# Kernel optimization log

Measured on AMD Instinct MI355X. Metric: run time of the kernel, lower is better.

Reference implementation:

```python
import jax, jax.numpy as jnp
import numpy as np

N, M, G, H, ND, E = 4096, 8192, 8, 128, 16, 131072
MAX_PERIOD = 10000.0


def setup_inputs() -> dict:
    key = jax.random.key(0)
    ks = jax.random.split(key, 24)
    s = 0.05
    inp = {
        "x": jax.random.normal(ks[0], (N, ND), jnp.float32),
        "edge_index": jax.random.randint(ks[1], (2, E), 0, N),
        "timestep": jax.random.randint(ks[2], (G,), 0, 1000),
        "batch_map": jnp.sort(jax.random.randint(ks[3], (N,), 0, G)),
        "obj_nucleotide_mask": jax.random.randint(ks[4], (M,), 0, 3),
        "obj_central_mask": jax.random.bernoulli(ks[5], 0.3, (M,)),
        "obj_backbone_mask": jax.random.bernoulli(ks[6], 0.5, (M,)),
        "obj_x": jax.random.normal(ks[7], (M, ND - 3), jnp.float32),
        "obj_pos": jax.random.normal(ks[8], (M, 3), jnp.float32),
        "obj_batch": jnp.sort(jax.random.randint(ks[9], (M,), 0, G)),
        # params (stored [in, out]; y = x @ W + b)
        "W_node": s * jax.random.normal(ks[10], (ND, H)),
        "b_node": jnp.zeros((H,)),
        "W_cond": s * jax.random.normal(ks[11], (H, H)),
        "b_cond": jnp.zeros((H,)),
        "W_time": s * jax.random.normal(ks[12], (H, H)),
        "b_time": jnp.zeros((H,)),
        "W_conv1": s * jax.random.normal(ks[13], (H, H)),
        "b_conv1": jnp.zeros((H,)),
        "W_conv2": s * jax.random.normal(ks[14], (H, H)),
        "b_conv2": jnp.zeros((H,)),
        "W_out": s * jax.random.normal(ks[15], (H, ND)),
        "b_out": jnp.zeros((ND,)),
        "w_edge": s * jax.random.normal(ks[16], (2 * H,)),
        "b_edge": jnp.zeros(()),
    }
    return inp


def timestep_embedding(t, dim):
    half = dim // 2
    freqs = jnp.exp(-np.log(MAX_PERIOD) * jnp.arange(half, dtype=jnp.float32) / half)
    args = t[:, None].astype(jnp.float32) * freqs[None]
    return jnp.concatenate([jnp.cos(args), jnp.sin(args)], axis=-1)


def gcn_conv(xh, src, dst, norm, W, b, n):
    # x' = D^-1/2 (A+I) D^-1/2 (X W) + b  (PyG GCNConv, self-loops included in src/dst/norm)
    xw = xh @ W
    msg = xw[src] * norm[:, None]
    return jax.ops.segment_sum(msg, dst, num_segments=n) + b


def reference(x, edge_index, timestep, batch_map, obj_nucleotide_mask,
              obj_central_mask, obj_backbone_mask, obj_x, obj_pos, obj_batch,
              W_node, b_node, W_cond, b_cond, W_time, b_time,
              W_conv1, b_conv1, W_conv2, b_conv2, W_out, b_out, w_edge, b_edge):
    n = x.shape[0]
    # timestep embedding + projections
    time_emb = timestep_embedding(timestep, H)            # [G, H]
    node_emb = x @ W_node + b_node                        # [N, H]

    # condition node pooling (masked mean per graph)
    is_left = obj_nucleotide_mask == 0
    is_central = obj_central_mask
    is_right = obj_nucleotide_mask == 2
    is_base = ~obj_backbone_mask
    is_cond = is_left | (is_central & is_base) | (is_right & is_base)  # [M]
    cond_x = jnp.concatenate([obj_x, obj_pos], axis=1)    # [M, ND]
    cond_emb = cond_x @ W_node + b_node                   # [M, H]
    cm = is_cond.astype(cond_emb.dtype)
    sums = jax.ops.segment_sum(cond_emb * cm[:, None], obj_batch, num_segments=G)
    cnt = jax.ops.segment_sum(cm, obj_batch, num_segments=G)
    pooled = sums / jnp.maximum(cnt, 1.0)[:, None]        # [G, H]

    time_h = time_emb @ W_time + b_time                   # [G, H]
    cond_h = pooled @ W_cond + b_cond                     # [G, H]
    node_emb = node_emb + time_h[batch_map] + cond_h[batch_map]

    # GCN normalization with self-loops (shared by both conv layers)
    loop = jnp.arange(n)
    src = jnp.concatenate([edge_index[0], loop])
    dst = jnp.concatenate([edge_index[1], loop])
    deg = jax.ops.segment_sum(jnp.ones_like(src, jnp.float32), dst, num_segments=n)
    dinv = jnp.where(deg > 0, jax.lax.rsqrt(jnp.maximum(deg, 1.0)), 0.0)
    norm = dinv[src] * dinv[dst]

    h = jax.nn.relu(gcn_conv(node_emb, src, dst, norm, W_conv1, b_conv1, n))
    h = jax.nn.relu(gcn_conv(h, src, dst, norm, W_conv2, b_conv2, n))

    node_noise_pred = h @ W_out + b_out                   # [N, ND]

    # all-pairs edge logits: cat([h[row], h[col]]) @ w_edge + b
    # == (h @ w_left)[row] + (h @ w_right)[col] + b  (same math, avoids [P, 2H])
    row, col = jnp.triu_indices(n, k=1)
    s_l = h @ w_edge[:H]
    s_r = h @ w_edge[H:]
    edge_logits = s_l[row] + s_r[col] + b_edge            # [N*(N-1)/2]
    return (node_noise_pred, edge_logits)
```

## Files before the change

### kernel.cpp

```cpp
#include <hip/hip_runtime.h>

#define NN 4096
#define MM 8192
#define GG 8
#define HH 128
#define NDD 16
#define EE 131072
#define CBLK 64
#define COBJ (MM / CBLK)
#define WBLK 8
#define SBLK 128
#define CAP 96

typedef float nt_f4 __attribute__((ext_vector_type(4)));

__global__ __launch_bounds__(1024) void k_zero(int* __restrict__ cnt) {
    ((int4*)cnt)[threadIdx.x] = make_int4(0, 0, 0, 0);
}

__global__ __launch_bounds__(256) void k_front(
    const float* __restrict__ obj_x, const float* __restrict__ obj_pos,
    const int* __restrict__ nuc, const int* __restrict__ central,
    const int* __restrict__ backbone, const int* __restrict__ obj_batch,
    const int* __restrict__ e_src, const int* __restrict__ e_dst,
    int* __restrict__ cnt, int* __restrict__ col_idx,
    float* __restrict__ partial, float* __restrict__ pcnt,
    const float* __restrict__ Wn, const float* __restrict__ Wc1,
    float* __restrict__ W1p) {
    int b = blockIdx.x, t = threadIdx.x;
    if (b < CBLK) {
        __shared__ float ls[GG * NDD];
        __shared__ float lc[GG];
        if (t < GG * NDD) ls[t] = 0.f;
        if (t < GG) lc[t] = 0.f;
        __syncthreads();
        int d = t & 15, oi = t >> 4;
        int base = b * COBJ;
#pragma unroll
        for (int pass = 0; pass < COBJ / 16; pass++) {
            int o = base + pass * 16 + oi;
            int nv = nuc[o];
            bool isb = (backbone[o] == 0);
            bool cond = (nv == 0) || ((central[o] != 0) && isb) || ((nv == 2) && isb);
            if (cond) {
                float v = (d < 13) ? obj_x[o * 13 + d] : obj_pos[o * 3 + (d - 13)];
                int g = obj_batch[o];
                atomicAdd(&ls[g * NDD + d], v);
                if (d == 0) atomicAdd(&lc[g], 1.f);
            }
        }
        __syncthreads();
        if (t < GG * NDD) partial[b * (GG * NDD) + t] = ls[t];
        if (t < GG) pcnt[b * GG + t] = lc[t];
        return;
    }
    if (b < CBLK + WBLK) {
        int wb = b - CBLK;
        int j = t & 127, a0 = t >> 7;
        int a = wb * 2 + a0;
        float acc = 0.f;
        for (int k = 0; k < HH; k++) acc += Wn[a * HH + k] * Wc1[k * HH + j];
        W1p[a * HH + j] = acc;
        return;
    }
    int sb = b - (CBLK + WBLK);
    int i4 = sb * 256 + t;
    int4 d4 = ((const int4*)e_dst)[i4];
    int4 s4 = ((const int4*)e_src)[i4];
    int p;
    p = atomicAdd(&cnt[d4.x], 1); if (p < CAP) col_idx[d4.x * CAP + p] = s4.x;
    p = atomicAdd(&cnt[d4.y], 1); if (p < CAP) col_idx[d4.y * CAP + p] = s4.y;
    p = atomicAdd(&cnt[d4.z], 1); if (p < CAP) col_idx[d4.z * CAP + p] = s4.z;
    p = atomicAdd(&cnt[d4.w], 1); if (p < CAP) col_idx[d4.w * CAP + p] = s4.w;
}

__global__ __launch_bounds__(1024) void k_mid(
    const int* __restrict__ timestep, const float* __restrict__ partial,
    const float* __restrict__ pcnt, const float* __restrict__ Wn,
    const float* __restrict__ bn, const float* __restrict__ Wt,
    const float* __restrict__ bt, const float* __restrict__ Wc,
    const float* __restrict__ bc, const float* __restrict__ Wc1,
    const float* __restrict__ x, const float* __restrict__ W1p,
    const int* __restrict__ bm, const int* __restrict__ cnt,
    float* __restrict__ xw) {
    int b = blockIdx.x, t = threadIdx.x;
    int g = t >> 7, j = t & 127;
    __shared__ float s16[GG * NDD];
    __shared__ float cinv[GG];
    __shared__ float te[GG * HH];
    __shared__ float pool[GG * HH];
    __shared__ float v2[GG * HH];
    __shared__ float c1s[GG * HH];
    __shared__ float xt[32 * NDD];
    {
        float tv = (float)timestep[g];
        float val;
        if (j < 64) {
            float f = expf(-logf(10000.f) * (float)j / 64.f);
            val = cosf(tv * f);
        } else {
            float f = expf(-logf(10000.f) * (float)(j - 64) / 64.f);
            val = sinf(tv * f);
        }
        te[t] = val;
    }
    if (t < GG * NDD) {
        float s = 0.f;
        for (int q = 0; q < CBLK; q++) s += partial[q * (GG * NDD) + t];
        s16[t] = s;
    } else if (t < GG * NDD + GG) {
        int gg = t - GG * NDD;
        float c = 0.f;
        for (int q = 0; q < CBLK; q++) c += pcnt[q * GG + gg];
        cinv[gg] = 1.f / fmaxf(c, 1.f);
    }
    if (t >= 512) xt[t - 512] = x[b * 32 * NDD + (t - 512)];
    __syncthreads();
    {
        float p = bn[j];
        float ci = cinv[g];
#pragma unroll
        for (int d = 0; d < NDD; d++) p += s16[g * NDD + d] * ci * Wn[d * HH + j];
        pool[t] = p;
    }
    __syncthreads();
    {
        float acc = bt[j] + bc[j] + bn[j];
#pragma unroll 4
        for (int k = 0; k < HH; k++)
            acc += te[g * HH + k] * Wt[k * HH + j] + pool[g * HH + k] * Wc[k * HH + j];
        v2[t] = acc;
    }
    __syncthreads();
    {
        float cc = 0.f;
#pragma unroll 4
        for (int k = 0; k < HH; k++) cc += v2[g * HH + k] * Wc1[k * HH + j];
        c1s[t] = cc;
    }
    __syncthreads();
    {
        int col = j, rh = g;
        int r0 = b * 32;
        float acc[4] = {0.f, 0.f, 0.f, 0.f};
#pragma unroll
        for (int k = 0; k < NDD; k++) {
            float wv = W1p[k * HH + col];
#pragma unroll
            for (int i = 0; i < 4; i++) acc[i] += xt[(rh * 4 + i) * NDD + k] * wv;
        }
#pragma unroll
        for (int i = 0; i < 4; i++) {
            int row = r0 + rh * 4 + i;
            int gr = bm[row];
            float dd = rsqrtf((float)cnt[row] + 1.f);
            xw[row * HH + col] = (acc[i] + c1s[gr * HH + col]) * dd;
        }
    }
}

__global__ __launch_bounds__(256) void k_conv1(
    const float* __restrict__ xw, const int* __restrict__ cnt,
    const int* __restrict__ col_idx, const float* __restrict__ b1,
    const float* __restrict__ Wc2, float* __restrict__ xw2) {
    int w = threadIdx.x >> 6, l = threadIdx.x & 63;
    int dst = blockIdx.x * 4 + w;
    int deg = cnt[dst];
    float dd = rsqrtf((float)deg + 1.f);
    int end = deg < CAP ? deg : CAP;
    const float2* xwp = (const float2*)xw;
    float2 acc = xwp[dst * 64 + l];
    const int* ci = col_idx + dst * CAP;
    int e = 0;
    for (; e + 7 < end; e += 8) {
        int s0 = ci[e], s1 = ci[e + 1], s2 = ci[e + 2], s3 = ci[e + 3];
        int s4 = ci[e + 4], s5 = ci[e + 5], s6 = ci[e + 6], s7 = ci[e + 7];
        float2 v0 = xwp[s0 * 64 + l], v1 = xwp[s1 * 64 + l];
        float2 v2 = xwp[s2 * 64 + l], v3 = xwp[s3 * 64 + l];
        float2 v4 = xwp[s4 * 64 + l], v5 = xwp[s5 * 64 + l];
        float2 v6 = xwp[s6 * 64 + l], v7 = xwp[s7 * 64 + l];
        acc.x += ((v0.x + v1.x) + (v2.x + v3.x)) + ((v4.x + v5.x) + (v6.x + v7.x));
        acc.y += ((v0.y + v1.y) + (v2.y + v3.y)) + ((v4.y + v5.y) + (v6.y + v7.y));
    }
    for (; e + 3 < end; e += 4) {
        int s0 = ci[e], s1 = ci[e + 1], s2 = ci[e + 2], s3 = ci[e + 3];
        float2 v0 = xwp[s0 * 64 + l], v1 = xwp[s1 * 64 + l];
        float2 v2 = xwp[s2 * 64 + l], v3 = xwp[s3 * 64 + l];
        acc.x += (v0.x + v1.x) + (v2.x + v3.x);
        acc.y += (v0.y + v1.y) + (v2.y + v3.y);
    }
    for (; e < end; e++) {
        float2 v = xwp[ci[e] * 64 + l];
        acc.x += v.x;
        acc.y += v.y;
    }
    float2 h;
    h.x = fmaxf(dd * acc.x + b1[2 * l], 0.f);
    h.y = fmaxf(dd * acc.y + b1[2 * l + 1], 0.f);
    __shared__ float hr[4][HH];
    __shared__ float wsm[64 * HH];
    *(float2*)&hr[w][2 * l] = h;
    float2 o = {0.f, 0.f};
#pragma unroll
    for (int half = 0; half < 2; half++) {
        __syncthreads();
        const float4* src4 = (const float4*)(Wc2 + half * 64 * HH);
        float4* dst4 = (float4*)wsm;
#pragma unroll
        for (int i = 0; i < (64 * HH / 4) / 256; i++)
            dst4[i * 256 + threadIdx.x] = src4[i * 256 + threadIdx.x];
        __syncthreads();
#pragma unroll 4
        for (int k = 0; k < 64; k++) {
            float hk = hr[w][half * 64 + k];
            float2 wv = *(const float2*)&wsm[k * HH + 2 * l];
            o.x += hk * wv.x;
            o.y += hk * wv.y;
        }
    }
    o.x *= dd;
    o.y *= dd;
    ((float2*)xw2)[dst * 64 + l] = o;
}

__global__ __launch_bounds__(256) void k_conv2_head(
    const float* __restrict__ xw, const int* __restrict__ cnt,
    const int* __restrict__ col_idx, const float* __restrict__ b2,
    const float* __restrict__ Wo, const float* __restrict__ bo,
    const float* __restrict__ we, float* __restrict__ out_pred,
    float* __restrict__ sl, float* __restrict__ sr) {
    int w = threadIdx.x >> 6, l = threadIdx.x & 63;
    int dst = blockIdx.x * 4 + w;
    int deg = cnt[dst];
    float dd = rsqrtf((float)deg + 1.f);
    int end = deg < CAP ? deg : CAP;
    const float2* xwp = (const float2*)xw;
    float2 acc = xwp[dst * 64 + l];
    const int* ci = col_idx + dst * CAP;
    int e = 0;
    for (; e + 7 < end; e += 8) {
        int s0 = ci[e], s1 = ci[e + 1], s2 = ci[e + 2], s3 = ci[e + 3];
        int s4 = ci[e + 4], s5 = ci[e + 5], s6 = ci[e + 6], s7 = ci[e + 7];
        float2 v0 = xwp[s0 * 64 + l], v1 = xwp[s1 * 64 + l];
        float2 v2 = xwp[s2 * 64 + l], v3 = xwp[s3 * 64 + l];
        float2 v4 = xwp[s4 * 64 + l], v5 = xwp[s5 * 64 + l];
        float2 v6 = xwp[s6 * 64 + l], v7 = xwp[s7 * 64 + l];
        acc.x += ((v0.x + v1.x) + (v2.x + v3.x)) + ((v4.x + v5.x) + (v6.x + v7.x));
        acc.y += ((v0.y + v1.y) + (v2.y + v3.y)) + ((v4.y + v5.y) + (v6.y + v7.y));
    }
    for (; e + 3 < end; e += 4) {
        int s0 = ci[e], s1 = ci[e + 1], s2 = ci[e + 2], s3 = ci[e + 3];
        float2 v0 = xwp[s0 * 64 + l], v1 = xwp[s1 * 64 + l];
        float2 v2 = xwp[s2 * 64 + l], v3 = xwp[s3 * 64 + l];
        acc.x += (v0.x + v1.x) + (v2.x + v3.x);
        acc.y += (v0.y + v1.y) + (v2.y + v3.y);
    }
    for (; e < end; e++) {
        float2 v = xwp[ci[e] * 64 + l];
        acc.x += v.x;
        acc.y += v.y;
    }
    float2 h;
    h.x = fmaxf(dd * acc.x + b2[2 * l], 0.f);
    h.y = fmaxf(dd * acc.y + b2[2 * l + 1], 0.f);
    __shared__ float hr[4][HH];
    *(float2*)&hr[w][2 * l] = h;
    __syncthreads();
    {
        int c = l & 15, p = l >> 4;
        float a = 0.f;
#pragma unroll 4
        for (int k = p * 32; k < p * 32 + 32; k++) a += hr[w][k] * Wo[k * NDD + c];
        a += __shfl_xor(a, 16);
        a += __shfl_xor(a, 32);
        if (p == 0) out_pred[dst * NDD + c] = a + bo[c];
    }
    {
        float h0 = hr[w][l], h1v = hr[w][64 + l];
        float pl = h0 * we[l] + h1v * we[64 + l];
        float pr = h0 * we[HH + l] + h1v * we[HH + 64 + l];
        for (int off = 32; off; off >>= 1) {
            pl += __shfl_down(pl, off);
            pr += __shfl_down(pr, off);
        }
        if (l == 0) {
            sl[dst] = pl;
            sr[dst] = pr;
        }
    }
}

__global__ __launch_bounds__(256) void k_edges(const float* __restrict__ sl,
                                               const float* __restrict__ sr,
                                               const float* __restrict__ be_p,
                                               float* __restrict__ out) {
    int b = blockIdx.x, t = threadIdx.x;
    float be = be_p[0];
#pragma unroll
    for (int half = 0; half < 2; half++) {
        int r = half == 0 ? b : (NN - 2 - b);
        int off = r * (2 * NN - r - 1) / 2;
        int len = NN - 1 - r;
        float s = sl[r] + be;
        const float* sp = sr + r + 1;
        float* op = out + off;
        int hd = (4 - (off & 3)) & 3;
        if (hd > len) hd = len;
        if (t < hd) __builtin_nontemporal_store(s + sp[t], op + t);
        int body = (len - hd) >> 2;
        float* opb = op + hd;
        const float* spb = sp + hd;
        for (int i = t; i < body; i += 256) {
            int base = 4 * i;
            nt_f4 v;
            v.x = s + spb[base];
            v.y = s + spb[base + 1];
            v.z = s + spb[base + 2];
            v.w = s + spb[base + 3];
            __builtin_nontemporal_store(v, (nt_f4*)(opb + base));
        }
        int tail = hd + body * 4;
        int rem = len - tail;
        if (t < rem) __builtin_nontemporal_store(s + sp[tail + t], op + tail + t);
    }
}

extern "C" void kernel_launch(void* const* d_in, const int* in_sizes, int n_in,
                              void* d_out, int out_size, void* d_ws, size_t ws_size,
                              hipStream_t stream) {
    const float* x = (const float*)d_in[0];
    const int* e_src = (const int*)d_in[1];
    const int* e_dst = e_src + EE;
    const int* timestep = (const int*)d_in[2];
    const int* batch_map = (const int*)d_in[3];
    const int* nuc = (const int*)d_in[4];
    const int* central = (const int*)d_in[5];
    const int* backbone = (const int*)d_in[6];
    const float* obj_x = (const float*)d_in[7];
    const float* obj_pos = (const float*)d_in[8];
    const int* obj_batch = (const int*)d_in[9];
    const float* W_node = (const float*)d_in[10];
    const float* b_node = (const float*)d_in[11];
    const float* W_cond = (const float*)d_in[12];
    const float* b_cond = (const float*)d_in[13];
    const float* W_time = (const float*)d_in[14];
    const float* b_time = (const float*)d_in[15];
    const float* W_conv1 = (const float*)d_in[16];
    const float* b_conv1 = (const float*)d_in[17];
    const float* W_conv2 = (const float*)d_in[18];
    const float* b_conv2 = (const float*)d_in[19];
    const float* W_out = (const float*)d_in[20];
    const float* b_out = (const float*)d_in[21];
    const float* w_edge = (const float*)d_in[22];
    const float* b_edge = (const float*)d_in[23];

    float* ws = (float*)d_ws;
    float* bufA = ws;
    float* bufB = bufA + NN * HH;
    float* W1p = bufB + NN * HH;
    float* partial = W1p + NDD * HH;
    float* pcnt = partial + CBLK * GG * NDD;
    float* sl = pcnt + CBLK * GG;
    float* sr = sl + NN;
    int* cnt = (int*)(sr + NN);
    int* col_idx = cnt + NN;

    float* out_pred = (float*)d_out;
    float* out_edges = out_pred + NN * NDD;

    k_zero<<<1, 1024, 0, stream>>>(cnt);
    k_front<<<CBLK + WBLK + SBLK, 256, 0, stream>>>(obj_x, obj_pos, nuc, central,
                                                    backbone, obj_batch, e_src, e_dst,
                                                    cnt, col_idx, partial, pcnt,
                                                    W_node, W_conv1, W1p);
    k_mid<<<NN / 32, 1024, 0, stream>>>(timestep, partial, pcnt, W_node, b_node,
                                        W_time, b_time, W_cond, b_cond, W_conv1,
                                        x, W1p, batch_map, cnt, bufA);
    k_conv1<<<NN / 4, 256, 0, stream>>>(bufA, cnt, col_idx, b_conv1, W_conv2, bufB);
    k_conv2_head<<<NN / 4, 256, 0, stream>>>(bufB, cnt, col_idx, b_conv2, W_out,
                                             b_out, w_edge, out_pred, sl, sr);
    k_edges<<<NN / 2, 256, 0, stream>>>(sl, sr, b_edge, out_edges);
}
```

Measured before the change: 176.9 us.

## Fold zeroing into front kernel, move CSR build into mid, split aggregation across two waves

Removes the separate zero-fill launch by zeroing degree counters inside the front kernel, and moves the edge-bucketing atomics into the mid kernel so xw no longer needs the degree scaling before counts exist. Source normalization is now applied per neighbor in conv1 via an extra cnt lookup and rsqrt. Both conv kernels now use two wavefronts per destination node, each summing half the neighbors and combining through shared memory, to raise parallelism on the gather. This adds per-edge cnt gathers and extra syncs in exchange for more parallelism and one fewer launch.

```diff
diff --git a/kernel.cpp b/kernel.cpp
--- a/kernel.cpp
+++ b/kernel.cpp
@@ -6,36 +6,36 @@
 #define HH 128
 #define NDD 16
 #define EE 131072
+#define ZBLK 4
 #define CBLK 64
 #define COBJ (MM / CBLK)
 #define WBLK 8
-#define SBLK 128
+#define SB2 32
 #define CAP 96
 
 typedef float nt_f4 __attribute__((ext_vector_type(4)));
-
-__global__ __launch_bounds__(1024) void k_zero(int* __restrict__ cnt) {
-    ((int4*)cnt)[threadIdx.x] = make_int4(0, 0, 0, 0);
-}
 
 __global__ __launch_bounds__(256) void k_front(
     const float* __restrict__ obj_x, const float* __restrict__ obj_pos,
     const int* __restrict__ nuc, const int* __restrict__ central,
     const int* __restrict__ backbone, const int* __restrict__ obj_batch,
-    const int* __restrict__ e_src, const int* __restrict__ e_dst,
-    int* __restrict__ cnt, int* __restrict__ col_idx,
-    float* __restrict__ partial, float* __restrict__ pcnt,
+    int* __restrict__ cnt, float* __restrict__ partial, float* __restrict__ pcnt,
     const float* __restrict__ Wn, const float* __restrict__ Wc1,
     float* __restrict__ W1p) {
     int b = blockIdx.x, t = threadIdx.x;
-    if (b < CBLK) {
+    if (b < ZBLK) {
+        ((int4*)cnt)[b * 256 + t] = make_int4(0, 0, 0, 0);
+        return;
+    }
+    if (b < ZBLK + CBLK) {
+        int cb = b - ZBLK;
         __shared__ float ls[GG * NDD];
         __shared__ float lc[GG];
         if (t < GG * NDD) ls[t] = 0.f;
         if (t < GG) lc[t] = 0.f;
         __syncthreads();
         int d = t & 15, oi = t >> 4;
-        int base = b * COBJ;
+        int base = cb * COBJ;
 #pragma unroll
         for (int pass = 0; pass < COBJ / 16; pass++) {
             int o = base + pass * 16 + oi;
@@ -50,40 +50,40 @@
             }
         }
         __syncthreads();
-        if (t < GG * NDD) partial[b * (GG * NDD) + t] = ls[t];
-        if (t < GG) pcnt[b * GG + t] = lc[t];
+        if (t < GG * NDD) partial[cb * (GG * NDD) + t] = ls[t];
+        if (t < GG) pcnt[cb * GG + t] = lc[t];
         return;
     }
-    if (b < CBLK + WBLK) {
-        int wb = b - CBLK;
-        int j = t & 127, a0 = t >> 7;
-        int a = wb * 2 + a0;
-        float acc = 0.f;
-        for (int k = 0; k < HH; k++) acc += Wn[a * HH + k] * Wc1[k * HH + j];
-        W1p[a * HH + j] = acc;
-        return;
-    }
-    int sb = b - (CBLK + WBLK);
-    int i4 = sb * 256 + t;
-    int4 d4 = ((const int4*)e_dst)[i4];
-    int4 s4 = ((const int4*)e_src)[i4];
-    int p;
-    p = atomicAdd(&cnt[d4.x], 1); if (p < CAP) col_idx[d4.x * CAP + p] = s4.x;
-    p = atomicAdd(&cnt[d4.y], 1); if (p < CAP) col_idx[d4.y * CAP + p] = s4.y;
-    p = atomicAdd(&cnt[d4.z], 1); if (p < CAP) col_idx[d4.z * CAP + p] = s4.z;
-    p = atomicAdd(&cnt[d4.w], 1); if (p < CAP) col_idx[d4.w * CAP + p] = s4.w;
+    int wb = b - (ZBLK + CBLK);
+    int j = t & 127, a = wb * 2 + (t >> 7);
+    float acc = 0.f;
+    for (int k = 0; k < HH; k++) acc += Wn[a * HH + k] * Wc1[k * HH + j];
+    W1p[a * HH + j] = acc;
 }
 
 __global__ __launch_bounds__(1024) void k_mid(
+    const int* __restrict__ e_src, const int* __restrict__ e_dst,
+    int* __restrict__ cnt, int* __restrict__ col_idx,
     const int* __restrict__ timestep, const float* __restrict__ partial,
     const float* __restrict__ pcnt, const float* __restrict__ Wn,
     const float* __restrict__ bn, const float* __restrict__ Wt,
     const float* __restrict__ bt, const float* __restrict__ Wc,
     const float* __restrict__ bc, const float* __restrict__ Wc1,
     const float* __restrict__ x, const float* __restrict__ W1p,
-    const int* __restrict__ bm, const int* __restrict__ cnt,
-    float* __restrict__ xw) {
+    const int* __restrict__ bm, float* __restrict__ xw) {
     int b = blockIdx.x, t = threadIdx.x;
+    if (b < SB2) {
+        int i4 = b * 1024 + t;
+        int4 d4 = ((const int4*)e_dst)[i4];
+        int4 s4 = ((const int4*)e_src)[i4];
+        int q;
+        q = atomicAdd(&cnt[d4.x], 1); if (q < CAP) col_idx[d4.x * CAP + q] = s4.x;
+        q = atomicAdd(&cnt[d4.y], 1); if (q < CAP) col_idx[d4.y * CAP + q] = s4.y;
+        q = atomicAdd(&cnt[d4.z], 1); if (q < CAP) col_idx[d4.z * CAP + q] = s4.z;
+        q = atomicAdd(&cnt[d4.w], 1); if (q < CAP) col_idx[d4.w * CAP + q] = s4.w;
+        return;
+    }
+    int rb = b - SB2;
     int g = t >> 7, j = t & 127;
     __shared__ float s16[GG * NDD];
     __shared__ float cinv[GG];
@@ -114,7 +114,7 @@
         for (int q = 0; q < CBLK; q++) c += pcnt[q * GG + gg];
         cinv[gg] = 1.f / fmaxf(c, 1.f);
     }
-    if (t >= 512) xt[t - 512] = x[b * 32 * NDD + (t - 512)];
+    if (t >= 512) xt[t - 512] = x[rb * 32 * NDD + (t - 512)];
     __syncthreads();
     {
         float p = bn[j];
@@ -141,7 +141,7 @@
     __syncthreads();
     {
         int col = j, rh = g;
-        int r0 = b * 32;
+        int r0 = rb * 32;
         float acc[4] = {0.f, 0.f, 0.f, 0.f};
 #pragma unroll
         for (int k = 0; k < NDD; k++) {
@@ -152,131 +152,148 @@
 #pragma unroll
         for (int i = 0; i < 4; i++) {
             int row = r0 + rh * 4 + i;
-            int gr = bm[row];
-            float dd = rsqrtf((float)cnt[row] + 1.f);
-            xw[row * HH + col] = (acc[i] + c1s[gr * HH + col]) * dd;
-        }
-    }
-}
-
-__global__ __launch_bounds__(256) void k_conv1(
+            xw[row * HH + col] = acc[i] + c1s[bm[row] * HH + col];
+        }
+    }
+}
+
+__global__ __launch_bounds__(256, 8) void k_conv1(
     const float* __restrict__ xw, const int* __restrict__ cnt,
     const int* __restrict__ col_idx, const float* __restrict__ b1,
     const float* __restrict__ Wc2, float* __restrict__ xw2) {
-    int w = threadIdx.x >> 6, l = threadIdx.x & 63;
-    int dst = blockIdx.x * 4 + w;
+    int t = threadIdx.x;
+    int w = t >> 6, l = t & 63;
+    int d = w >> 1, half = w & 1;
+    int dst = blockIdx.x * 2 + d;
     int deg = cnt[dst];
     float dd = rsqrtf((float)deg + 1.f);
     int end = deg < CAP ? deg : CAP;
+    int mid = end >> 1;
     const float2* xwp = (const float2*)xw;
-    float2 acc = xwp[dst * 64 + l];
     const int* ci = col_idx + dst * CAP;
-    int e = 0;
-    for (; e + 7 < end; e += 8) {
+    float2 acc = {0.f, 0.f};
+    if (half == 0) {
+        float2 sv = xwp[dst * 64 + l];
+        acc.x = dd * sv.x;
+        acc.y = dd * sv.y;
+    }
+    int e = half ? mid : 0;
+    int e1 = half ? end : mid;
+    for (; e + 3 < e1; e += 4) {
         int s0 = ci[e], s1 = ci[e + 1], s2 = ci[e + 2], s3 = ci[e + 3];
-        int s4 = ci[e + 4], s5 = ci[e + 5], s6 = ci[e + 6], s7 = ci[e + 7];
+        float r0 = rsqrtf((float)cnt[s0] + 1.f), r1 = rsqrtf((float)cnt[s1] + 1.f);
+        float r2 = rsqrtf((float)cnt[s2] + 1.f), r3 = rsqrtf((float)cnt[s3] + 1.f);
         float2 v0 = xwp[s0 * 64 + l], v1 = xwp[s1 * 64 + l];
         float2 v2 = xwp[s2 * 64 + l], v3 = xwp[s3 * 64 + l];
-        float2 v4 = xwp[s4 * 64 + l], v5 = xwp[s5 * 64 + l];
-        float2 v6 = xwp[s6 * 64 + l], v7 = xwp[s7 * 64 + l];
-        acc.x += ((v0.x + v1.x) + (v2.x + v3.x)) + ((v4.x + v5.x) + (v6.x + v7.x));
-        acc.y += ((v0.y + v1.y) + (v2.y + v3.y)) + ((v4.y + v5.y) + (v6.y + v7.y));
-    }
-    for (; e + 3 < end; e += 4) {
+        acc.x += (r0 * v0.x + r1 * v1.x) + (r2 * v2.x + r3 * v3.x);
+        acc.y += (r0 * v0.y + r1 * v1.y) + (r2 * v2.y + r3 * v3.y);
+    }
+    for (; e < e1; e++) {
+        int s = ci[e];
+        float r = rsqrtf((float)cnt[s] + 1.f);
+        float2 v = xwp[s * 64 + l];
+        acc.x += r * v.x;
+        acc.y += r * v.y;
+    }
+    __shared__ float hr[2][HH];
+    __shared__ float2 part[2][64];
+    __shared__ float wsm[32 * HH];
+    if (half == 1) part[d][l] = acc;
+    __syncthreads();
+    if (half == 0) {
+        float2 pv = part[d][l];
+        acc.x += pv.x;
+        acc.y += pv.y;
+        float2 h;
+        h.x = fmaxf(dd * acc.x + b1[2 * l], 0.f);
+        h.y = fmaxf(dd * acc.y + b1[2 * l + 1], 0.f);
+        *(float2*)&hr[d][2 * l] = h;
+    }
+    float2 o = {0.f, 0.f};
+#pragma unroll
+    for (int q = 0; q < 4; q++) {
+        __syncthreads();
+        const float4* s4 = (const float4*)(Wc2 + q * 32 * HH);
+        float4* d4 = (float4*)wsm;
+#pragma unroll
+        for (int i = 0; i < 4; i++) d4[i * 256 + t] = s4[i * 256 + t];
+        __syncthreads();
+#pragma unroll 4
+        for (int k = 0; k < 16; k++) {
+            int kk = half * 16 + k;
+            float hk = hr[d][q * 32 + kk];
+            float2 wv = *(const float2*)&wsm[kk * HH + 2 * l];
+            o.x += hk * wv.x;
+            o.y += hk * wv.y;
+        }
+    }
+    __syncthreads();
+    if (half == 1) part[d][l] = o;
+    __syncthreads();
+    if (half == 0) {
+        float2 pv = part[d][l];
+        o.x = (o.x + pv.x) * dd;
+        o.y = (o.y + pv.y) * dd;
+        ((float2*)xw2)[dst * 64 + l] = o;
+    }
+}
+
+__global__ __launch_bounds__(256, 8) void k_conv2_head(
+    const float* __restrict__ xw, const int* __restrict__ cnt,
+    const int* __restrict__ col_idx, const float* __restrict__ b2,
+    const float* __restrict__ Wo, const float* __restrict__ bo,
+    const float* __restrict__ we, float* __restrict__ out_pred,
+    float* __restrict__ sl, float* __restrict__ sr) {
+    int t = threadIdx.x;
+    int w = t >> 6, l = t & 63;
+    int d = w >> 1, half = w & 1;
+    int dst = blockIdx.x * 2 + d;
+    int deg = cnt[dst];
+    float dd = rsqrtf((float)deg + 1.f);
+    int end = deg < CAP ? deg : CAP;
+    int mid = end >> 1;
+    const float2* xwp = (const float2*)xw;
+    const int* ci = col_idx + dst * CAP;
+    float2 acc = {0.f, 0.f};
+    if (half == 0) acc = xwp[dst * 64 + l];
+    int e = half ? mid : 0;
+    int e1 = half ? end : mid;
+    for (; e + 3 < e1; e += 4) {
         int s0 = ci[e], s1 = ci[e + 1], s2 = ci[e + 2], s3 = ci[e + 3];
         float2 v0 = xwp[s0 * 64 + l], v1 = xwp[s1 * 64 + l];
         float2 v2 = xwp[s2 * 64 + l], v3 = xwp[s3 * 64 + l];
         acc.x += (v0.x + v1.x) + (v2.x + v3.x);
         acc.y += (v0.y + v1.y) + (v2.y + v3.y);
     }
-    for (; e < end; e++) {
+    for (; e < e1; e++) {
         float2 v = xwp[ci[e] * 64 + l];
         acc.x += v.x;
         acc.y += v.y;
     }
-    float2 h;
-    h.x = fmaxf(dd * acc.x + b1[2 * l], 0.f);
-    h.y = fmaxf(dd * acc.y + b1[2 * l + 1], 0.f);
-    __shared__ float hr[4][HH];
-    __shared__ float wsm[64 * HH];
-    *(float2*)&hr[w][2 * l] = h;
-    float2 o = {0.f, 0.f};
-#pragma unroll
-    for (int half = 0; half < 2; half++) {
-        __syncthreads();
-        const float4* src4 = (const float4*)(Wc2 + half * 64 * HH);
-        float4* dst4 = (float4*)wsm;
-#pragma unroll
-        for (int i = 0; i < (64 * HH / 4) / 256; i++)
-            dst4[i * 256 + threadIdx.x] = src4[i * 256 + threadIdx.x];
-        __syncthreads();
-#pragma unroll 4
-        for (int k = 0; k < 64; k++) {
-            float hk = hr[w][half * 64 + k];
-            float2 wv = *(const float2*)&wsm[k * HH + 2 * l];
-            o.x += hk * wv.x;
-            o.y += hk * wv.y;
-        }
-    }
-    o.x *= dd;
-    o.y *= dd;
-    ((float2*)xw2)[dst * 64 + l] = o;
-}
-
-__global__ __launch_bounds__(256) void k_conv2_head(
-    const float* __restrict__ xw, const int* __restrict__ cnt,
-    const int* __restrict__ col_idx, const float* __restrict__ b2,
-    const float* __restrict__ Wo, const float* __restrict__ bo,
-    const float* __restrict__ we, float* __restrict__ out_pred,
-    float* __restrict__ sl, float* __restrict__ sr) {
-    int w = threadIdx.x >> 6, l = threadIdx.x & 63;
-    int dst = blockIdx.x * 4 + w;
-    int deg = cnt[dst];
-    float dd = rsqrtf((float)deg + 1.f);
-    int end = deg < CAP ? deg : CAP;
-    const float2* xwp = (const float2*)xw;
-    float2 acc = xwp[dst * 64 + l];
-    const int* ci = col_idx + dst * CAP;
-    int e = 0;
-    for (; e + 7 < end; e += 8) {
-        int s0 = ci[e], s1 = ci[e + 1], s2 = ci[e + 2], s3 = ci[e + 3];
-        int s4 = ci[e + 4], s5 = ci[e + 5], s6 = ci[e + 6], s7 = ci[e + 7];
-        float2 v0 = xwp[s0 * 64 + l], v1 = xwp[s1 * 64 + l];
-        float2 v2 = xwp[s2 * 64 + l], v3 = xwp[s3 * 64 + l];
-        float2 v4 = xwp[s4 * 64 + l], v5 = xwp[s5 * 64 + l];
-        float2 v6 = xwp[s6 * 64 + l], v7 = xwp[s7 * 64 + l];
-        acc.x += ((v0.x + v1.x) + (v2.x + v3.x)) + ((v4.x + v5.x) + (v6.x + v7.x));
-        acc.y += ((v0.y + v1.y) + (v2.y + v3.y)) + ((v4.y + v5.y) + (v6.y + v7.y));
-    }
-    for (; e + 3 < end; e += 4) {
-        int s0 = ci[e], s1 = ci[e + 1], s2 = ci[e + 2], s3 = ci[e + 3];
-        float2 v0 = xwp[s0 * 64 + l], v1 = xwp[s1 * 64 + l];
-        float2 v2 = xwp[s2 * 64 + l], v3 = xwp[s3 * 64 + l];
-        acc.x += (v0.x + v1.x) + (v2.x + v3.x);
-        acc.y += (v0.y + v1.y) + (v2.y + v3.y);
-    }
-    for (; e < end; e++) {
-        float2 v = xwp[ci[e] * 64 + l];
-        acc.x += v.x;
-        acc.y += v.y;
-    }
-    float2 h;
-    h.x = fmaxf(dd * acc.x + b2[2 * l], 0.f);
-    h.y = fmaxf(dd * acc.y + b2[2 * l + 1], 0.f);
-    __shared__ float hr[4][HH];
-    *(float2*)&hr[w][2 * l] = h;
-    __syncthreads();
-    {
-        int c = l & 15, p = l >> 4;
+    __shared__ float hr[2][HH];
+    __shared__ float2 part[2][64];
+    if (half == 1) part[d][l] = acc;
+    __syncthreads();
+    if (half == 0) {
+        float2 pv = part[d][l];
+        acc.x += pv.x;
+        acc.y += pv.y;
+        float2 h;
+        h.x = fmaxf(dd * acc.x + b2[2 * l], 0.f);
+        h.y = fmaxf(dd * acc.y + b2[2 * l + 1], 0.f);
+        *(float2*)&hr[d][2 * l] = h;
+    }
+    __syncthreads();
+    if (half == 0) {
+        int c = l & 15, pp = l >> 4;
         float a = 0.f;
 #pragma unroll 4
-        for (int k = p * 32; k < p * 32 + 32; k++) a += hr[w][k] * Wo[k * NDD + c];
+        for (int k = pp * 32; k < pp * 32 + 32; k++) a += hr[d][k] * Wo[k * NDD + c];
         a += __shfl_xor(a, 16);
         a += __shfl_xor(a, 32);
-        if (p == 0) out_pred[dst * NDD + c] = a + bo[c];
-    }
-    {
-        float h0 = hr[w][l], h1v = hr[w][64 + l];
+        if (pp == 0) out_pred[dst * NDD + c] = a + bo[c];
+    } else {
+        float h0 = hr[d][l], h1v = hr[d][64 + l];
         float pl = h0 * we[l] + h1v * we[64 + l];
         float pr = h0 * we[HH + l] + h1v * we[HH + 64 + l];
         for (int off = 32; off; off >>= 1) {
@@ -368,16 +385,15 @@
     float* out_pred = (float*)d_out;
     float* out_edges = out_pred + NN * NDD;
 
-    k_zero<<<1, 1024, 0, stream>>>(cnt);
-    k_front<<<CBLK + WBLK + SBLK, 256, 0, stream>>>(obj_x, obj_pos, nuc, central,
-                                                    backbone, obj_batch, e_src, e_dst,
-                                                    cnt, col_idx, partial, pcnt,
-                                                    W_node, W_conv1, W1p);
-    k_mid<<<NN / 32, 1024, 0, stream>>>(timestep, partial, pcnt, W_node, b_node,
-                                        W_time, b_time, W_cond, b_cond, W_conv1,
-                                        x, W1p, batch_map, cnt, bufA);
-    k_conv1<<<NN / 4, 256, 0, stream>>>(bufA, cnt, col_idx, b_conv1, W_conv2, bufB);
-    k_conv2_head<<<NN / 4, 256, 0, stream>>>(bufB, cnt, col_idx, b_conv2, W_out,
+    k_front<<<ZBLK + CBLK + WBLK, 256, 0, stream>>>(obj_x, obj_pos, nuc, central,
+                                                    backbone, obj_batch, cnt, partial,
+                                                    pcnt, W_node, W_conv1, W1p);
+    k_mid<<<SB2 + NN / 32, 1024, 0, stream>>>(e_src, e_dst, cnt, col_idx, timestep,
+                                              partial, pcnt, W_node, b_node, W_time,
+                                              b_time, W_cond, b_cond, W_conv1, x,
+                                              W1p, batch_map, bufA);
+    k_conv1<<<NN / 2, 256, 0, stream>>>(bufA, cnt, col_idx, b_conv1, W_conv2, bufB);
+    k_conv2_head<<<NN / 2, 256, 0, stream>>>(bufB, cnt, col_idx, b_conv2, W_out,
                                              b_out, w_edge, out_pred, sl, sr);
     k_edges<<<NN / 2, 256, 0, stream>>>(sl, sr, b_edge, out_edges);
 }
```

Result: faster. 172.8 us (-2.3%).
